# Performance work log

Hardware: AMD Instinct MI355X
Metric: run time of the kernel (lower is better)

## Reference

```python
import jax, jax.numpy as jnp
import numpy as np

L1, L2 = 16, 16            # lattice shape -> translation group
N_SYMM = L1 * L2           # 256 group elements
IN_FEATURES = 32
FEATURES = 64
BATCH = 16


def translation_table(l1, l2):
    """Product table pt[g, h] = index of g^{-1} h for the 2D translation group."""
    n = l1 * l2
    g = np.arange(n)
    a, b = g // l2, g % l2          # coords of g
    c, d = a, b                     # coords of h (same enumeration)
    pt = ((c[None, :] - a[:, None]) % l1) * l2 + ((d[None, :] - b[:, None]) % l2)
    return jnp.asarray(pt, dtype=jnp.int32)  # (n_symm, n_symm)


def setup_inputs() -> dict:
    key = jax.random.key(0)
    kx, kk, kb = jax.random.split(key, 3)
    x = jax.random.normal(kx, (BATCH, IN_FEATURES, N_SYMM), dtype=jnp.float32)
    # default_equivariant_initializer ~ lecun normal, fan_in = in_features * kernel_size
    scale = 1.0 / np.sqrt(IN_FEATURES * N_SYMM)
    kernel = scale * jax.random.normal(kk, (FEATURES, IN_FEATURES, N_SYMM), dtype=jnp.float32)
    bias = jnp.zeros((FEATURES,), dtype=jnp.float32)
    product_table = translation_table(L1, L2)
    return {"x": x, "kernel": kernel, "bias": bias, "product_table": product_table}


def reference(x, kernel, bias, product_table):
    # Expand kernel via group product table: K[f, i, g, h] = kernel[f, i, pt[g, h]]
    # (feature_group_count = 1, mask = None so unmask is identity, kernel_size = n_symm)
    K = jnp.take(kernel, product_table, axis=2)          # (F, I, S, S) -- 536 MB fp32
    # dot_general contracts x dims (in_features, n_symm) with K dims (I, first S)
    out = jnp.einsum('big,figh->bfh', x, K)              # (B, F, S)
    out = out + bias[:, None]                            # bias broadcast over group dim
    return out
```

## Files before the change

kernel.cpp:

```cpp
#include <hip/hip_runtime.h>

typedef unsigned short u16;
typedef unsigned int u32;
typedef __attribute__((ext_vector_type(8))) short bfx8;
typedef __attribute__((ext_vector_type(4))) float fx4;
typedef __attribute__((ext_vector_type(4))) u32 ux4;
typedef __attribute__((ext_vector_type(2))) u32 ux2;

__device__ inline u32 f2bf(float v) {
  u32 u = __builtin_bit_cast(u32, v);
  u = (u + 0x7fffu + ((u >> 16) & 1u)) >> 16;
  return u;
}

__global__ __launch_bounds__(512, 1) void eq_main(const float* __restrict__ xin,
                                                  const float* __restrict__ kin,
                                                  float* __restrict__ part) {
  __shared__ u16 As[32768];
  __shared__ u32 P[1024];
  __shared__ u16 xraw[512];
  __shared__ float red[4 * 64 * 68];

  const int b = blockIdx.x & 15;
  const int ich = blockIdx.x >> 4;
  const int t = threadIdx.x;

  if (t < 128) {
    int iLoc = t >> 6, s4 = (t & 63) << 2;
    fx4 v = *(const fx4*)(xin + ((b << 5) + (ich << 1) + iLoc) * 256 + s4);
    ux2 p;
    p[0] = f2bf(v[0]) | (f2bf(v[1]) << 16);
    p[1] = f2bf(v[2]) | (f2bf(v[3]) << 16);
    *(ux2*)(xraw + iLoc * 256 + s4) = p;
  }

#pragma unroll
  for (int it = 0; it < 8; ++it) {
    int slot = it * 512 + t;
    int iLoc = slot >> 11;
    int f = (slot >> 5) & 63;
    int c = slot & 31;
    int cs = c ^ (f & 31);
    const float* src = kin + f * 8192 + ((ich << 1) + iLoc) * 256 + (cs << 3);
    fx4 v0 = *(const fx4*)src;
    fx4 v1 = *(const fx4*)(src + 4);
    ux4 p;
    p[0] = f2bf(v0[0]) | (f2bf(v0[1]) << 16);
    p[1] = f2bf(v0[2]) | (f2bf(v0[3]) << 16);
    p[2] = f2bf(v1[0]) | (f2bf(v1[1]) << 16);
    p[3] = f2bf(v1[2]) | (f2bf(v1[3]) << 16);
    *(ux4*)(As + slot * 8) = p;
  }
  __syncthreads();

  {
    int iLoc = t >> 8, tt = t & 255;
    int r = tt >> 4, u = tt & 15;
    int c0 = (32 - 2 * u) & 15;
    int c1 = (c0 + 15) & 15;
    int c2 = (c0 + 14) & 15;
    const u16* xr = xraw + iLoc * 256 + r * 16;
    u32 va = xr[c0], vb = xr[c1], vc = xr[c2];
    P[iLoc * 512 + r * 32 + u] = va | (vb << 16);
    P[iLoc * 512 + r * 32 + 16 + u] = vb | (vc << 16);
  }
  __syncthreads();

  const int lane = t & 63;
  const int w = t >> 6;
  const int iLoc = w >> 2;
  const int wq = w & 3;
  const int n = lane & 15;
  const int quad = lane >> 4;
  const int s2_0 = (quad & 1) << 3;
  const int par = n & 1;
  const int u0 = ((s2_0 - n - par) & 15) >> 1;
  const int Pb = iLoc * 512 + (par << 4) + u0;
  const int s1q = quad >> 1;
  const u16* Aw = As + (iLoc << 14);

  fx4 acc[4][4];
#pragma unroll
  for (int a = 0; a < 4; ++a)
#pragma unroll
    for (int c = 0; c < 4; ++c) acc[a][c] = (fx4){0.f, 0.f, 0.f, 0.f};

#pragma unroll
  for (int kstep = 0; kstep < 8; ++kstep) {
    bfx8 af[4];
#pragma unroll
    for (int ft = 0; ft < 4; ++ft) {
      int f = (ft << 4) + n;
      int ch = ((kstep << 2) + quad) ^ (f & 31);
      af[ft] = *(const bfx8*)(Aw + f * 256 + ch * 8);
    }
    const int s1 = (kstep << 1) + s1q;
    bfx8 bfr[4];
#pragma unroll
    for (int ht = 0; ht < 4; ++ht) {
      int r = ((wq << 2) + ht - s1) & 15;
      int idx = r * 32 + Pb;
      ux4 bv = {P[idx], P[idx + 1], P[idx + 2], P[idx + 3]};
      bfr[ht] = __builtin_bit_cast(bfx8, bv);
    }
#pragma unroll
    for (int ft = 0; ft < 4; ++ft)
#pragma unroll
      for (int ht = 0; ht < 4; ++ht)
        acc[ft][ht] =
            __builtin_amdgcn_mfma_f32_16x16x32_bf16(af[ft], bfr[ht], acc[ft][ht], 0, 0, 0);
  }

  if (w >= 4) {
#pragma unroll
    for (int ft = 0; ft < 4; ++ft)
#pragma unroll
      for (int ht = 0; ht < 4; ++ht) {
        float* pr = &red[wq * 4352 + (ht * 16 + n) * 68 + (ft << 4) + (quad << 2)];
        *(fx4*)pr = acc[ft][ht];
      }
  }
  __syncthreads();
  if (w < 4) {
    float* pw = part + (((ich << 4) + b) << 14);
#pragma unroll
    for (int ft = 0; ft < 4; ++ft)
#pragma unroll
      for (int ht = 0; ht < 4; ++ht) {
        const float* pr = &red[wq * 4352 + (ht * 16 + n) * 68 + (ft << 4) + (quad << 2)];
        fx4 vv = *(const fx4*)pr;
        acc[ft][ht] = acc[ft][ht] + vv;
#pragma unroll
        for (int reg = 0; reg < 4; ++reg) {
          int f = (ft << 4) + (quad << 2) + reg;
          int h = (wq << 6) + (ht << 4) + n;
          pw[f * 256 + h] = acc[ft][ht][reg];
        }
      }
  }
}

__global__ __launch_bounds__(256) void eq_reduce(const float* __restrict__ part,
                                                 const float* __restrict__ bias,
                                                 float* __restrict__ out) {
  int o = (blockIdx.x * 256 + threadIdx.x) * 4;
  fx4 s = {0.f, 0.f, 0.f, 0.f};
#pragma unroll
  for (int i = 0; i < 16; ++i) s = s + *(const fx4*)(part + i * 262144 + o);
  float bv = bias[(o >> 8) & 63];
  s = s + (fx4){bv, bv, bv, bv};
  *(fx4*)(out + o) = s;
}

extern "C" void kernel_launch(void* const* d_in, const int* in_sizes, int n_in,
                              void* d_out, int out_size, void* d_ws, size_t ws_size,
                              hipStream_t stream) {
  (void)in_sizes; (void)n_in; (void)out_size; (void)ws_size;
  const float* x = (const float*)d_in[0];
  const float* k = (const float*)d_in[1];
  const float* bias = (const float*)d_in[2];
  float* part = (float*)d_ws;
  float* out = (float*)d_out;

  eq_main<<<256, 512, 0, stream>>>(x, k, part);
  eq_reduce<<<256, 256, 0, stream>>>(part, bias, out);
}
```

Measured before the change: 73.46 us.

## Store partials as bf16, replicate x rows in LDS, coalesce partial writes

```diff
diff --git a/kernel.cpp b/kernel.cpp
--- a/kernel.cpp
+++ b/kernel.cpp
@@ -12,13 +12,15 @@
   u = (u + 0x7fffu + ((u >> 16) & 1u)) >> 16;
   return u;
 }
+__device__ inline float bflo(u32 v) { return __builtin_bit_cast(float, v << 16); }
+__device__ inline float bfhi(u32 v) { return __builtin_bit_cast(float, v & 0xffff0000u); }
 
 __global__ __launch_bounds__(512, 1) void eq_main(const float* __restrict__ xin,
                                                   const float* __restrict__ kin,
-                                                  float* __restrict__ part) {
+                                                  u16* __restrict__ part) {
   __shared__ u16 As[32768];
-  __shared__ u32 P[1024];
   __shared__ u16 xraw[512];
+  __shared__ u16 Xrep[4096];
   __shared__ float red[4 * 64 * 68];
 
   const int b = blockIdx.x & 15;
@@ -26,58 +28,54 @@
   const int t = threadIdx.x;
 
   if (t < 128) {
-    int iLoc = t >> 6, s4 = (t & 63) << 2;
-    fx4 v = *(const fx4*)(xin + ((b << 5) + (ich << 1) + iLoc) * 256 + s4);
+    int iL = t >> 6, s4 = (t & 63) << 2;
+    fx4 v = *(const fx4*)(xin + ((b << 5) + (ich << 1) + iL) * 256 + s4);
     ux2 p;
     p[0] = f2bf(v[0]) | (f2bf(v[1]) << 16);
     p[1] = f2bf(v[2]) | (f2bf(v[3]) << 16);
-    *(ux2*)(xraw + iLoc * 256 + s4) = p;
+    *(ux2*)(xraw + iL * 256 + s4) = p;
   }
 
 #pragma unroll
   for (int it = 0; it < 8; ++it) {
     int slot = it * 512 + t;
-    int iLoc = slot >> 11;
+    int iL = slot >> 11;
     int f = (slot >> 5) & 63;
     int c = slot & 31;
     int cs = c ^ (f & 31);
-    const float* src = kin + f * 8192 + ((ich << 1) + iLoc) * 256 + (cs << 3);
+    const float* src = kin + f * 8192 + ((ich << 1) + iL) * 256 + (cs << 3);
     fx4 v0 = *(const fx4*)src;
     fx4 v1 = *(const fx4*)(src + 4);
     ux4 p;
-    p[0] = f2bf(v0[0]) | (f2bf(v0[1]) << 16);
-    p[1] = f2bf(v0[2]) | (f2bf(v0[3]) << 16);
-    p[2] = f2bf(v1[0]) | (f2bf(v1[1]) << 16);
-    p[3] = f2bf(v1[2]) | (f2bf(v1[3]) << 16);
+    p[0] = f2bf(v1[3]) | (f2bf(v1[2]) << 16);
+    p[1] = f2bf(v1[1]) | (f2bf(v1[0]) << 16);
+    p[2] = f2bf(v0[3]) | (f2bf(v0[2]) << 16);
+    p[3] = f2bf(v0[1]) | (f2bf(v0[0]) << 16);
     *(ux4*)(As + slot * 8) = p;
   }
   __syncthreads();
 
   {
-    int iLoc = t >> 8, tt = t & 255;
-    int r = tt >> 4, u = tt & 15;
-    int c0 = (32 - 2 * u) & 15;
-    int c1 = (c0 + 15) & 15;
-    int c2 = (c0 + 14) & 15;
-    const u16* xr = xraw + iLoc * 256 + r * 16;
-    u32 va = xr[c0], vb = xr[c1], vc = xr[c2];
-    P[iLoc * 512 + r * 32 + u] = va | (vb << 16);
-    P[iLoc * 512 + r * 32 + 16 + u] = vb | (vc << 16);
+    int triple = t >> 1;
+    int iL = triple >> 7, r = (triple >> 3) & 15, q = triple & 7;
+    int th = (t & 1) * 8;
+    const u16* xr = xraw + iL * 256 + r * 16;
+    u16* xd = Xrep + ((iL * 16 + r) * 8 + q) * 16 + th;
+#pragma unroll
+    for (int j = 0; j < 8; ++j) xd[j] = xr[(th + j + q) & 15];
   }
   __syncthreads();
 
   const int lane = t & 63;
   const int w = t >> 6;
-  const int iLoc = w >> 2;
+  const int iL = w >> 2;
   const int wq = w & 3;
   const int n = lane & 15;
   const int quad = lane >> 4;
-  const int s2_0 = (quad & 1) << 3;
-  const int par = n & 1;
-  const int u0 = ((s2_0 - n - par) & 15) >> 1;
-  const int Pb = iLoc * 512 + (par << 4) + u0;
   const int s1q = quad >> 1;
-  const u16* Aw = As + (iLoc << 14);
+  const int c0 = (n - ((quad & 1) << 3) + 9) & 15;
+  const int XB = iL * 2048 + (c0 & 7) * 16 + (c0 & 8);
+  const u16* Aw = As + (iL << 14);
 
   fx4 acc[4][4];
 #pragma unroll
@@ -99,9 +97,7 @@
 #pragma unroll
     for (int ht = 0; ht < 4; ++ht) {
       int r = ((wq << 2) + ht - s1) & 15;
-      int idx = r * 32 + Pb;
-      ux4 bv = {P[idx], P[idx + 1], P[idx + 2], P[idx + 3]};
-      bfr[ht] = __builtin_bit_cast(bfx8, bv);
+      bfr[ht] = *(const bfx8*)(Xrep + XB + r * 128);
     }
 #pragma unroll
     for (int ft = 0; ft < 4; ++ft)
@@ -112,44 +108,67 @@
   }
 
   if (w >= 4) {
+    float* rb = red + wq * 4352;
 #pragma unroll
     for (int ft = 0; ft < 4; ++ft)
 #pragma unroll
-      for (int ht = 0; ht < 4; ++ht) {
-        float* pr = &red[wq * 4352 + (ht * 16 + n) * 68 + (ft << 4) + (quad << 2)];
-        *(fx4*)pr = acc[ft][ht];
-      }
+      for (int ht = 0; ht < 4; ++ht)
+#pragma unroll
+        for (int reg = 0; reg < 4; ++reg)
+          rb[((ft << 4) + (quad << 2) + reg) * 68 + (ht << 4) + n] = acc[ft][ht][reg];
   }
   __syncthreads();
   if (w < 4) {
-    float* pw = part + (((ich << 4) + b) << 14);
+    float* rb = red + wq * 4352;
 #pragma unroll
     for (int ft = 0; ft < 4; ++ft)
 #pragma unroll
-      for (int ht = 0; ht < 4; ++ht) {
-        const float* pr = &red[wq * 4352 + (ht * 16 + n) * 68 + (ft << 4) + (quad << 2)];
-        fx4 vv = *(const fx4*)pr;
-        acc[ft][ht] = acc[ft][ht] + vv;
+      for (int ht = 0; ht < 4; ++ht)
 #pragma unroll
         for (int reg = 0; reg < 4; ++reg) {
-          int f = (ft << 4) + (quad << 2) + reg;
-          int h = (wq << 6) + (ht << 4) + n;
-          pw[f * 256 + h] = acc[ft][ht][reg];
+          int idx = ((ft << 4) + (quad << 2) + reg) * 68 + (ht << 4) + n;
+          rb[idx] += acc[ft][ht][reg];
         }
-      }
+  }
+  __syncthreads();
+  {
+    u16* pw = part + (((ich << 4) + b) << 14);
+#pragma unroll
+    for (int it = 0; it < 4; ++it) {
+      int task = it * 512 + t;
+      int f = task >> 5, o = task & 31;
+      const float* rr = red + (o >> 3) * 4352 + f * 68 + (o & 7) * 8;
+      fx4 v0 = *(const fx4*)rr;
+      fx4 v1 = *(const fx4*)(rr + 4);
+      ux4 p;
+      p[0] = f2bf(v0[0]) | (f2bf(v0[1]) << 16);
+      p[1] = f2bf(v0[2]) | (f2bf(v0[3]) << 16);
+      p[2] = f2bf(v1[0]) | (f2bf(v1[1]) << 16);
+      p[3] = f2bf(v1[2]) | (f2bf(v1[3]) << 16);
+      *(ux4*)(pw + f * 256 + o * 8) = p;
+    }
   }
 }
 
-__global__ __launch_bounds__(256) void eq_reduce(const float* __restrict__ part,
+__global__ __launch_bounds__(256) void eq_reduce(const u16* __restrict__ part,
                                                  const float* __restrict__ bias,
                                                  float* __restrict__ out) {
-  int o = (blockIdx.x * 256 + threadIdx.x) * 4;
-  fx4 s = {0.f, 0.f, 0.f, 0.f};
+  int o8 = (blockIdx.x * 256 + threadIdx.x) * 8;
+  float s[8] = {0.f, 0.f, 0.f, 0.f, 0.f, 0.f, 0.f, 0.f};
 #pragma unroll
-  for (int i = 0; i < 16; ++i) s = s + *(const fx4*)(part + i * 262144 + o);
-  float bv = bias[(o >> 8) & 63];
-  s = s + (fx4){bv, bv, bv, bv};
-  *(fx4*)(out + o) = s;
+  for (int c = 0; c < 16; ++c) {
+    ux4 v = *(const ux4*)(part + c * 262144 + o8);
+#pragma unroll
+    for (int d = 0; d < 4; ++d) {
+      s[2 * d] += bflo(v[d]);
+      s[2 * d + 1] += bfhi(v[d]);
+    }
+  }
+  float bv = bias[(o8 >> 8) & 63];
+  fx4 r0 = {s[0] + bv, s[1] + bv, s[2] + bv, s[3] + bv};
+  fx4 r1 = {s[4] + bv, s[5] + bv, s[6] + bv, s[7] + bv};
+  *(fx4*)(out + o8) = r0;
+  *(fx4*)(out + o8 + 4) = r1;
 }
 
 extern "C" void kernel_launch(void* const* d_in, const int* in_sizes, int n_in,
@@ -159,9 +178,9 @@
   const float* x = (const float*)d_in[0];
   const float* k = (const float*)d_in[1];
   const float* bias = (const float*)d_in[2];
-  float* part = (float*)d_ws;
+  u16* part = (u16*)d_ws;
   float* out = (float*)d_out;
 
   eq_main<<<256, 512, 0, stream>>>(x, k, part);
-  eq_reduce<<<256, 256, 0, stream>>>(part, bias, out);
+  eq_reduce<<<128, 256, 0, stream>>>(part, bias, out);
 }
```

New measurement: 74.34 us. About the same (+1.2%).
